# Kernel optimization log

Measured on AMD Instinct MI355X. Metric: run time of the kernel, lower is better.

## Reference

```python
import jax, jax.numpy as jnp
import numpy as np

DT_MIN, DT_MAX = 1e-3, 1e-1
LN_EPS = 1e-5


def layernorm(x, w, b):
    mu = jnp.mean(x, axis=-1, keepdims=True)
    var = jnp.mean(jnp.square(x - mu), axis=-1, keepdims=True)
    return (x - mu) * jax.lax.rsqrt(var + LN_EPS) * w + b


def _scan(Lam_bar, Bu, reverse=False):
    # Lam_bar: (P,) complex64; Bu: (B, L, P) complex64
    A = jnp.broadcast_to(Lam_bar, Bu.shape)

    def binop(e_i, e_j):
        a_i, b_i = e_i
        a_j, b_j = e_j
        return a_j * a_i, a_j * b_i + b_j

    _, xs = jax.lax.associative_scan(binop, (A, Bu), axis=1, reverse=reverse)
    return xs  # (B, L, P)


def s5_ssm(u, Lambda_re, Lambda_im, log_step, B_re, B_im, C_re, C_im, D):
    # u: (B, L, H) real. Diagonal S5 with ZOH discretization, bidirectional.
    step = jnp.exp(log_step)                          # (P,)
    Lam = (Lambda_re + 1j * Lambda_im).astype(jnp.complex64)
    Lam_bar = jnp.exp(Lam * step)                     # (P,)
    Bmat = (B_re + 1j * B_im).astype(jnp.complex64)   # (P, H)
    B_bar = ((Lam_bar - 1.0) / Lam)[:, None] * Bmat   # (P, H)
    Bu = jnp.einsum('blh,ph->blp', u.astype(jnp.complex64), B_bar)  # (B,L,P)
    xs_f = _scan(Lam_bar, Bu, reverse=False)
    xs_b = _scan(Lam_bar, Bu, reverse=True)
    xs = jnp.concatenate([xs_f, xs_b], axis=-1)       # (B, L, 2P)
    C = (C_re + 1j * C_im).astype(jnp.complex64)      # (H, 2P)
    ys = 2.0 * jnp.einsum('hp,blp->blh', C, xs).real  # conj-symmetric output
    return ys + D * u


def gelu(x):
    return jax.nn.gelu(x, approximate=False)  # torch default (erf) gelu


def s5_block(x, ln1_w, ln1_b, ln2_w, ln2_b, Lambda_re, Lambda_im, log_step,
             B_re, B_im, C_re, C_im, D, ff_enc_w, ff_dec_w):
    # attention-style half: pre-LN + S5 + gelu + residual (residual = normed input)
    fx = layernorm(x, ln1_w, ln1_b)
    res = fx
    x = gelu(s5_ssm(fx, Lambda_re, Lambda_im, log_step, B_re, B_im, C_re, C_im, D)) + res
    # FFN half: pre-LN + GEGLU + residual (residual = normed input)
    fx = layernorm(x, ln2_w, ln2_b)
    res = fx
    h = fx @ ff_enc_w.T                               # (B, L, 2*dim)
    a, g = jnp.split(h, 2, axis=-1)
    x = (a * gelu(g)) @ ff_dec_w.T + res
    return x


def setup_inputs() -> dict:
    B, L, D_IN, DIM, P = 4, 4096, 512, 1024, 512
    key = jax.random.key(0)
    ks = jax.random.split(key, 16)
    inp = {}
    inp['x'] = jax.random.normal(ks[0], (B, L, D_IN), dtype=jnp.float32)
    inp['W_in'] = jax.random.normal(ks[1], (DIM, D_IN), jnp.float32) / np.sqrt(D_IN)
    inp['W_out'] = jax.random.normal(ks[2], (D_IN, DIM), jnp.float32) / np.sqrt(DIM)
    inp['ln1_w'] = jnp.ones((DIM,), jnp.float32)
    inp['ln1_b'] = jnp.zeros((DIM,), jnp.float32)
    inp['ln2_w'] = jnp.ones((DIM,), jnp.float32)
    inp['ln2_b'] = jnp.zeros((DIM,), jnp.float32)
    inp['Lambda_re'] = -0.5 * jnp.exp(jax.random.normal(ks[3], (P,), jnp.float32))
    inp['Lambda_im'] = jnp.pi * jax.random.normal(ks[4], (P,), jnp.float32)
    inp['log_step'] = jax.random.uniform(ks[5], (P,), jnp.float32,
                                         minval=np.log(DT_MIN), maxval=np.log(DT_MAX))
    inp['B_re'] = jax.random.normal(ks[6], (P, DIM), jnp.float32) / np.sqrt(DIM)
    inp['B_im'] = jax.random.normal(ks[7], (P, DIM), jnp.float32) / np.sqrt(DIM)
    inp['C_re'] = jax.random.normal(ks[8], (DIM, 2 * P), jnp.float32) / np.sqrt(2 * P)
    inp['C_im'] = jax.random.normal(ks[9], (DIM, 2 * P), jnp.float32) / np.sqrt(2 * P)
    inp['D'] = jax.random.normal(ks[10], (DIM,), jnp.float32)
    inp['ff_enc_w'] = jax.random.normal(ks[11], (2 * DIM, DIM), jnp.float32) / np.sqrt(DIM)
    inp['ff_dec_w'] = jax.random.normal(ks[12], (DIM, DIM), jnp.float32) / np.sqrt(DIM)
    return inp


def reference(x, W_in, W_out, ln1_w, ln1_b, ln2_w, ln2_b, Lambda_re, Lambda_im,
              log_step, B_re, B_im, C_re, C_im, D, ff_enc_w, ff_dec_w):
    h = x @ W_in.T                                    # (B, L, dim)
    h = s5_block(h, ln1_w, ln1_b, ln2_w, ln2_b, Lambda_re, Lambda_im, log_step,
                 B_re, B_im, C_re, C_im, D, ff_enc_w, ff_dec_w)
    return h @ W_out.T                                # (B, L, d_input)
```

## Files before the change

kernel.cpp:

```cpp
#include <hip/hip_runtime.h>
#include <cstdint>

typedef __bf16 bf16;
typedef __bf16 bf16x2 __attribute__((ext_vector_type(2)));
typedef __bf16 bf16x4 __attribute__((ext_vector_type(4)));
typedef __bf16 bf16x8 __attribute__((ext_vector_type(8)));
typedef float f32x4 __attribute__((ext_vector_type(4)));

#define MROWS 16384
#define DIMH 1024
#define PDIM 512
#define LSEQ 4096
#define CL 16
#define NC (LSEQ / CL)

typedef const __attribute__((address_space(1))) unsigned int* gas_t;
typedef __attribute__((address_space(3))) unsigned int* las_t;

__device__ __forceinline__ float gelu_f(float x) {
  return 0.5f * x * (1.0f + erff(x * 0.70710678118654752f));
}

__global__ __launch_bounds__(256) void k_mega(
    const float* __restrict__ x, const float* __restrict__ W_in,
    const float* __restrict__ W_out, const float* __restrict__ ffe,
    const float* __restrict__ ffd, const float* __restrict__ Lre,
    const float* __restrict__ Lim, const float* __restrict__ lstep,
    const float* __restrict__ Bre, const float* __restrict__ Bim,
    const float* __restrict__ Cre, const float* __restrict__ Cim,
    bf16* __restrict__ xb, bf16* __restrict__ winb, bf16* __restrict__ woutb,
    bf16* __restrict__ ffeb, bf16* __restrict__ ffdb, bf16* __restrict__ bcat,
    bf16* __restrict__ cc, float2* __restrict__ lamb) {
  const int bid = blockIdx.x;
  const int tid = threadIdx.x;
  auto cvt4 = [&](const float* src, bf16* dst, int i4) {
    const float4 v = *(const float4*)(src + i4);
    bf16x4 o = { (bf16)v.x, (bf16)v.y, (bf16)v.z, (bf16)v.w };
    *(bf16x4*)(dst + i4) = o;
  };
  if (bid < 8192) {
    cvt4(x, xb, bid * 1024 + tid * 4);
  } else if (bid < 8704) {
    cvt4(W_in, winb, (bid - 8192) * 1024 + tid * 4);
  } else if (bid < 9216) {
    cvt4(W_out, woutb, (bid - 8704) * 1024 + tid * 4);
  } else if (bid < 11264) {
    cvt4(ffe, ffeb, (bid - 9216) * 1024 + tid * 4);
  } else if (bid < 12288) {
    cvt4(ffd, ffdb, (bid - 11264) * 1024 + tid * 4);
  } else if (bid < 12800) {
    const int i4 = (bid - 12288) * 1024 + tid * 4;
    const int p = i4 >> 10;
    const float lre = Lre[p], lim = Lim[p];
    const float st = expf(lstep[p]);
    const float er = expf(lre * st);
    const float lbr = er * cosf(lim * st);
    const float lbi = er * sinf(lim * st);
    const float ar = lbr - 1.0f, ai = lbi;
    const float d = lre * lre + lim * lim;
    const float cx = (ar * lre + ai * lim) / d;
    const float cy = (ai * lre - ar * lim) / d;
    const float4 br = *(const float4*)(Bre + i4);
    const float4 bi = *(const float4*)(Bim + i4);
    bf16x4 o1 = { (bf16)(cx * br.x - cy * bi.x), (bf16)(cx * br.y - cy * bi.y),
                  (bf16)(cx * br.z - cy * bi.z), (bf16)(cx * br.w - cy * bi.w) };
    bf16x4 o2 = { (bf16)(cx * bi.x + cy * br.x), (bf16)(cx * bi.y + cy * br.y),
                  (bf16)(cx * bi.z + cy * br.z), (bf16)(cx * bi.w + cy * br.w) };
    *(bf16x4*)(bcat + i4) = o1;
    *(bf16x4*)(bcat + i4 + PDIM * DIMH) = o2;
  } else if (bid < 14848) {
    const int i4 = (bid - 12800) * 1024 + tid * 4;
    const int n = i4 >> 11, k0 = i4 & 2047;
    const float* src;
    float sgn;
    int kk;
    if (k0 < 512)       { src = Cre + n * 1024;       sgn =  2.0f; kk = k0; }
    else if (k0 < 1024) { src = Cim + n * 1024;       sgn = -2.0f; kk = k0 - 512; }
    else if (k0 < 1536) { src = Cre + n * 1024 + 512; sgn =  2.0f; kk = k0 - 1024; }
    else                { src = Cim + n * 1024 + 512; sgn = -2.0f; kk = k0 - 1536; }
    const float4 v = *(const float4*)(src + kk);
    bf16x4 o = { (bf16)(sgn * v.x), (bf16)(sgn * v.y), (bf16)(sgn * v.z), (bf16)(sgn * v.w) };
    *(bf16x4*)(cc + i4) = o;
  } else {
    const int p = (bid - 14848) * 256 + tid;
    if (p < PDIM) {
      const float lre = Lre[p], lim = Lim[p];
      const float st = expf(lstep[p]);
      const float er = expf(lre * st);
      lamb[p] = make_float2(er * cosf(lim * st), er * sinf(lim * st));
    }
  }
}


#define VMCNT4 asm volatile("s_waitcnt vmcnt(4)" ::: "memory")
#define VMCNT0 asm volatile("s_waitcnt vmcnt(0)" ::: "memory")
#define LGKM0  asm volatile("s_waitcnt lgkmcnt(0)" ::: "memory")
#define SCHED0 __builtin_amdgcn_sched_barrier(0)
#define BAR    __builtin_amdgcn_s_barrier()

#define PHASE(slot, kh, STAGE_STMT, WAIT_STMT)                                 \
  {                                                                            \
    ldB(slot, kh, bfr);                                                        \
    ldA(slot, kh, afr);                                                        \
    STAGE_STMT;                                                                \
    SCHED0;                                                                    \
    BAR;                                                                       \
    LGKM0;                                                                     \
    SCHED0;                                                                    \
    __builtin_amdgcn_s_setprio(1);                                             \
    _Pragma("unroll")                                                          \
    for (int m = 0; m < 4; ++m)                                                \
      _Pragma("unroll")                                                        \
      for (int n = 0; n < 4; ++n)                                              \
        acc[m][n] = __builtin_amdgcn_mfma_f32_16x16x32_bf16(                   \
            afr[m], bfr[n], acc[m][n], 0, 0, 0);                               \
    __builtin_amdgcn_s_setprio(0);                                             \
    SCHED0;                                                                    \
    WAIT_STMT;                                                                 \
    BAR;                                                                       \
  }

template <int EPI>
__global__ __launch_bounds__(256, 2) void k_gemm(const bf16* __restrict__ A,
                                                 const bf16* __restrict__ W,
                                                 float* __restrict__ Cf,
                                                 bf16* __restrict__ Cb,
                                                 const bf16* __restrict__ auxb,
                                                 int K, int N, int nbnl) {
  extern __shared__ char lds[];
  const int q = (int)gridDim.x >> 3;
  const int s = ((int)blockIdx.x & 7) * q + ((int)blockIdx.x >> 3);
  const int bm = s >> nbnl;
  const int bn = s & ((1 << nbnl) - 1);
  const int tid = threadIdx.x;
  const int lane = tid & 63;
  const int wave = tid >> 6;
  const int wr = wave >> 1;
  const int wc = wave & 1;

  const size_t arow0 = (size_t)bm * 128;
  const size_t wrow0 = (size_t)bn * 128;
  const int srow = tid >> 2;
  const int schunk = (tid & 3) ^ ((tid >> 3) & 3);
  const int wbase = wave << 10;

  f32x4 acc[4][4];
#pragma unroll
  for (int i = 0; i < 4; ++i)
#pragma unroll
    for (int j = 0; j < 4; ++j) acc[i][j] = (f32x4){0.f, 0.f, 0.f, 0.f};

  auto stage = [&](int slot, int kh, int kt) {
    const int kcol = kt * 64 + kh * 32 + schunk * 8;
    {
      char* base = lds + slot * 16384 + kh * 8192;
      __builtin_amdgcn_global_load_lds(
          (gas_t)(A + (arow0 + srow) * (size_t)K + kcol), (las_t)(base + wbase), 16, 0, 0);
      __builtin_amdgcn_global_load_lds(
          (gas_t)(A + (arow0 + 64 + srow) * (size_t)K + kcol), (las_t)(base + 4096 + wbase), 16, 0, 0);
    }
    {
      char* base = lds + 32768 + slot * 16384 + kh * 8192;
      __builtin_amdgcn_global_load_lds(
          (gas_t)(W + (wrow0 + srow) * (size_t)K + kcol), (las_t)(base + wbase), 16, 0, 0);
      __builtin_amdgcn_global_load_lds(
          (gas_t)(W + (wrow0 + 64 + srow) * (size_t)K + kcol), (las_t)(base + 4096 + wbase), 16, 0, 0);
    }
  };

  auto ldA = [&](int slot, int kh, bf16x8* af) {
#pragma unroll
    for (int m = 0; m < 4; ++m) {
      const int row = wr * 64 + m * 16 + (lane & 15);
      const int pc = (lane >> 4) ^ ((row >> 1) & 3);
      af[m] = *(const bf16x8*)(lds + slot * 16384 + kh * 8192 + row * 64 + pc * 16);
    }
  };
  auto ldB = [&](int slot, int kh, bf16x8* bf) {
#pragma unroll
    for (int n = 0; n < 4; ++n) {
      const int row = wc * 64 + n * 16 + (lane & 15);
      const int pc = (lane >> 4) ^ ((row >> 1) & 3);
      bf[n] = *(const bf16x8*)(lds + 32768 + slot * 16384 + kh * 8192 + row * 64 + pc * 16);
    }
  };

  bf16x8 afr[4], bfr[4];

  stage(0, 0, 0);
  stage(0, 1, 0);
  stage(1, 0, 1);
  VMCNT4;
  BAR;

  const int NT = K >> 7;
  for (int t = 0; t < NT; ++t) {
    const int nl = (t + 1 < NT);
    PHASE(0, 0, stage(1, 1, 2 * t + 1), (void)0);
    if (nl) { PHASE(0, 1, stage(0, 0, 2 * t + 2), VMCNT4); }
    else    { PHASE(0, 1, (void)0, VMCNT0); }
    PHASE(1, 0, if (nl) stage(0, 1, 2 * t + 2), (void)0);
    if (nl) { PHASE(1, 1, stage(1, 0, 2 * t + 3), VMCNT4); }
    else    { PHASE(1, 1, (void)0, (void)0); }
  }

  const int n0 = (int)wrow0 + wc * 64 + (lane & 15);
  const size_t m0 = arow0 + wr * 64 + ((lane >> 4) << 2);
#pragma unroll
  for (int mi = 0; mi < 4; ++mi)
#pragma unroll
    for (int n = 0; n < 4; ++n) {
      const size_t mb = m0 + mi * 16;
      const int nn = n0 + n * 16;
#pragma unroll
      for (int r = 0; r < 4; ++r) {
        const size_t idx = (mb + r) * (size_t)N + nn;
        const float v = acc[mi][n][r];
        if constexpr (EPI == 0) {
          Cf[idx] = v;
        } else if constexpr (EPI == 1) {
          Cb[idx] = (bf16)((float)auxb[idx] * gelu_f(v));
        } else if constexpr (EPI == 2) {
          Cb[idx] = (bf16)(v + (float)auxb[idx]);
        } else {
          Cb[idx] = (bf16)v;
        }
      }
    }
}

__global__ __launch_bounds__(256) void k_ln(const bf16* __restrict__ X,
                                            const float* __restrict__ w,
                                            const float* __restrict__ bb,
                                            bf16* __restrict__ Yb) {
  const int m = blockIdx.x;
  const int tid = threadIdx.x;
  const bf16x4 v4 = *(const bf16x4*)(X + (size_t)m * DIMH + tid * 4);
  const float v0 = (float)v4[0], v1 = (float)v4[1], v2 = (float)v4[2], v3 = (float)v4[3];
  float s = v0 + v1 + v2 + v3;
  float s2 = v0 * v0 + v1 * v1 + v2 * v2 + v3 * v3;
#pragma unroll
  for (int off = 32; off > 0; off >>= 1) { s += __shfl_down(s, off); s2 += __shfl_down(s2, off); }
  __shared__ float rs[4], rq[4];
  if ((tid & 63) == 0) { rs[tid >> 6] = s; rq[tid >> 6] = s2; }
  __syncthreads();
  s = rs[0] + rs[1] + rs[2] + rs[3];
  s2 = rq[0] + rq[1] + rq[2] + rq[3];
  const float mu = s * (1.0f / DIMH);
  const float inv = rsqrtf(s2 * (1.0f / DIMH) - mu * mu + 1e-5f);
  const float4 wv = ((const float4*)w)[tid];
  const float4 bv = ((const float4*)bb)[tid];
  bf16x4 ob = { (bf16)((v0 - mu) * inv * wv.x + bv.x), (bf16)((v1 - mu) * inv * wv.y + bv.y),
                (bf16)((v2 - mu) * inv * wv.z + bv.z), (bf16)((v3 - mu) * inv * wv.w + bv.w) };
  *(bf16x4*)(Yb + (size_t)m * DIMH + tid * 4) = ob;
}

__global__ __launch_bounds__(256) void k_ln2e(const bf16* __restrict__ YS,
                                              bf16* FXE,
                                              const float* __restrict__ Dv,
                                              const float* __restrict__ w,
                                              const float* __restrict__ bb) {
  const int m = blockIdx.x;
  const int tid = threadIdx.x;
  const bf16x4 ys4 = *(const bf16x4*)(YS + (size_t)m * DIMH + tid * 4);
  const bf16x4 fx4 = *(const bf16x4*)(FXE + (size_t)m * DIMH + tid * 4);
  const float4 dv = ((const float4*)Dv)[tid];
  const float f0 = (float)fx4[0], f1 = (float)fx4[1], f2 = (float)fx4[2], f3 = (float)fx4[3];
  const float t0 = gelu_f((float)ys4[0] + dv.x * f0) + f0;
  const float t1 = gelu_f((float)ys4[1] + dv.y * f1) + f1;
  const float t2 = gelu_f((float)ys4[2] + dv.z * f2) + f2;
  const float t3 = gelu_f((float)ys4[3] + dv.w * f3) + f3;
  float s = t0 + t1 + t2 + t3;
  float s2 = t0 * t0 + t1 * t1 + t2 * t2 + t3 * t3;
#pragma unroll
  for (int off = 32; off > 0; off >>= 1) { s += __shfl_down(s, off); s2 += __shfl_down(s2, off); }
  __shared__ float rs[4], rq[4];
  if ((tid & 63) == 0) { rs[tid >> 6] = s; rq[tid >> 6] = s2; }
  __syncthreads();
  s = rs[0] + rs[1] + rs[2] + rs[3];
  s2 = rq[0] + rq[1] + rq[2] + rq[3];
  const float mu = s * (1.0f / DIMH);
  const float inv = rsqrtf(s2 * (1.0f / DIMH) - mu * mu + 1e-5f);
  const float4 wv = ((const float4*)w)[tid];
  const float4 bv = ((const float4*)bb)[tid];
  bf16x4 ob = { (bf16)((t0 - mu) * inv * wv.x + bv.x), (bf16)((t1 - mu) * inv * wv.y + bv.y),
                (bf16)((t2 - mu) * inv * wv.z + bv.z), (bf16)((t3 - mu) * inv * wv.w + bv.w) };
  *(bf16x4*)(FXE + (size_t)m * DIMH + tid * 4) = ob;
}

__global__ __launch_bounds__(256) void k_scanA(const bf16* __restrict__ Bu,
                                               const float2* __restrict__ lamb,
                                               float2* __restrict__ carry) {
  const int bc = blockIdx.x;
  const int b = bc >> 8, c = bc & (NC - 1);
  const int t = threadIdx.x;
  const size_t rbase = ((size_t)b * LSEQ + (size_t)c * CL) * DIMH;
  float2 re[CL], im[CL];
#pragma unroll
  for (int i = 0; i < CL; ++i) {
    const bf16x2 r2 = *(const bf16x2*)(Bu + rbase + (size_t)i * DIMH + 2 * t);
    const bf16x2 i2 = *(const bf16x2*)(Bu + rbase + (size_t)i * DIMH + PDIM + 2 * t);
    re[i] = make_float2((float)r2[0], (float)r2[1]);
    im[i] = make_float2((float)i2[0], (float)i2[1]);
  }
  const float2 l0 = lamb[2 * t];
  const float2 l1 = lamb[2 * t + 1];
  const size_t cb = ((size_t)bc * 2) * PDIM;
  {
    float s0r = 0.f, s0i = 0.f, s1r = 0.f, s1i = 0.f;
#pragma unroll
    for (int i = 0; i < CL; ++i) {
      float nr = l0.x * s0r - l0.y * s0i + re[i].x;
      float ni = l0.x * s0i + l0.y * s0r + im[i].x;
      s0r = nr; s0i = ni;
      nr = l1.x * s1r - l1.y * s1i + re[i].y;
      ni = l1.x * s1i + l1.y * s1r + im[i].y;
      s1r = nr; s1i = ni;
    }
    carry[cb + 2 * t]     = make_float2(s0r, s0i);
    carry[cb + 2 * t + 1] = make_float2(s1r, s1i);
  }
  {
    float s0r = 0.f, s0i = 0.f, s1r = 0.f, s1i = 0.f;
#pragma unroll
    for (int i = CL - 1; i >= 0; --i) {
      float nr = l0.x * s0r - l0.y * s0i + re[i].x;
      float ni = l0.x * s0i + l0.y * s0r + im[i].x;
      s0r = nr; s0i = ni;
      nr = l1.x * s1r - l1.y * s1i + re[i].y;
      ni = l1.x * s1i + l1.y * s1r + im[i].y;
      s1r = nr; s1i = ni;
    }
    carry[cb + PDIM + 2 * t]     = make_float2(s0r, s0i);
    carry[cb + PDIM + 2 * t + 1] = make_float2(s1r, s1i);
  }
}

__global__ __launch_bounds__(256) void k_scanB(const float2* __restrict__ carry,
                                               const float2* __restrict__ lamb,
                                               float2* __restrict__ seed) {
  const int b = blockIdx.x;
  const int t = threadIdx.x;
  const float2 l0 = lamb[2 * t], l1 = lamb[2 * t + 1];
  float L0r = l0.x, L0i = l0.y, L1r = l1.x, L1i = l1.y;
#pragma unroll
  for (int q = 0; q < 4; ++q) {
    float tr = L0r * L0r - L0i * L0i; L0i = 2.f * L0r * L0i; L0r = tr;
    tr = L1r * L1r - L1i * L1i; L1i = 2.f * L1r * L1i; L1r = tr;
  }
  float S0r = 0.f, S0i = 0.f, S1r = 0.f, S1i = 0.f;
  for (int c = 0; c < NC; ++c) {
    const size_t base = (((size_t)b * NC + c) * 2) * PDIM;
    const float2 c0 = carry[base + 2 * t];
    const float2 c1 = carry[base + 2 * t + 1];
    seed[base + 2 * t]     = make_float2(S0r, S0i);
    seed[base + 2 * t + 1] = make_float2(S1r, S1i);
    float nr = L0r * S0r - L0i * S0i + c0.x;
    float ni = L0r * S0i + L0i * S0r + c0.y;
    S0r = nr; S0i = ni;
    nr = L1r * S1r - L1i * S1i + c1.x;
    ni = L1r * S1i + L1i * S1r + c1.y;
    S1r = nr; S1i = ni;
  }
  S0r = 0.f; S0i = 0.f; S1r = 0.f; S1i = 0.f;
  for (int c = NC - 1; c >= 0; --c) {
    const size_t base = (((size_t)b * NC + c) * 2) * PDIM + PDIM;
    const float2 c0 = carry[base + 2 * t];
    const float2 c1 = carry[base + 2 * t + 1];
    seed[base + 2 * t]     = make_float2(S0r, S0i);
    seed[base + 2 * t + 1] = make_float2(S1r, S1i);
    float nr = L0r * S0r - L0i * S0i + c0.x;
    float ni = L0r * S0i + L0i * S0r + c0.y;
    S0r = nr; S0i = ni;
    nr = L1r * S1r - L1i * S1i + c1.x;
    ni = L1r * S1i + L1i * S1r + c1.y;
    S1r = nr; S1i = ni;
  }
}

__global__ __launch_bounds__(256) void k_scanC(const bf16* __restrict__ Bu,
                                               const float2* __restrict__ lamb,
                                               const float2* __restrict__ seed,
                                               bf16* __restrict__ xs) {
  const int bc = blockIdx.x;
  const int b = bc >> 8, c = bc & (NC - 1);
  const int t = threadIdx.x;
  const size_t rbase = ((size_t)b * LSEQ + (size_t)c * CL) * DIMH;
  float2 re[CL], im[CL];
#pragma unroll
  for (int i = 0; i < CL; ++i) {
    const bf16x2 r2 = *(const bf16x2*)(Bu + rbase + (size_t)i * DIMH + 2 * t);
    const bf16x2 i2 = *(const bf16x2*)(Bu + rbase + (size_t)i * DIMH + PDIM + 2 * t);
    re[i] = make_float2((float)r2[0], (float)r2[1]);
    im[i] = make_float2((float)i2[0], (float)i2[1]);
  }
  const float2 l0 = lamb[2 * t];
  const float2 l1 = lamb[2 * t + 1];
  const size_t sb = ((size_t)bc * 2) * PDIM;
  const size_t obase = ((size_t)b * LSEQ + (size_t)c * CL) * 2048;
  {
    const float2 s0 = seed[sb + 2 * t];
    const float2 s1 = seed[sb + 2 * t + 1];
    float s0r = s0.x, s0i = s0.y, s1r = s1.x, s1i = s1.y;
#pragma unroll
    for (int i = 0; i < CL; ++i) {
      float nr = l0.x * s0r - l0.y * s0i + re[i].x;
      float ni = l0.x * s0i + l0.y * s0r + im[i].x;
      s0r = nr; s0i = ni;
      nr = l1.x * s1r - l1.y * s1i + re[i].y;
      ni = l1.x * s1i + l1.y * s1r + im[i].y;
      s1r = nr; s1i = ni;
      bf16x2 wr2 = { (bf16)s0r, (bf16)s1r };
      bf16x2 wi2 = { (bf16)s0i, (bf16)s1i };
      *(bf16x2*)(xs + obase + (size_t)i * 2048 + 2 * t) = wr2;
      *(bf16x2*)(xs + obase + (size_t)i * 2048 + PDIM + 2 * t) = wi2;
    }
  }
  {
    const float2 s0 = seed[sb + PDIM + 2 * t];
    const float2 s1 = seed[sb + PDIM + 2 * t + 1];
    float s0r = s0.x, s0i = s0.y, s1r = s1.x, s1i = s1.y;
#pragma unroll
    for (int i = CL - 1; i >= 0; --i) {
      float nr = l0.x * s0r - l0.y * s0i + re[i].x;
      float ni = l0.x * s0i + l0.y * s0r + im[i].x;
      s0r = nr; s0i = ni;
      nr = l1.x * s1r - l1.y * s1i + re[i].y;
      ni = l1.x * s1i + l1.y * s1r + im[i].y;
      s1r = nr; s1i = ni;
      bf16x2 wr2 = { (bf16)s0r, (bf16)s1r };
      bf16x2 wi2 = { (bf16)s0i, (bf16)s1i };
      *(bf16x2*)(xs + obase + (size_t)i * 2048 + 1024 + 2 * t) = wr2;
      *(bf16x2*)(xs + obase + (size_t)i * 2048 + 1536 + 2 * t) = wi2;
    }
  }
}

extern "C" void kernel_launch(void* const* d_in, const int* in_sizes, int n_in,
                              void* d_out, int out_size, void* d_ws, size_t ws_size,
                              hipStream_t stream) {
  const float* x    = (const float*)d_in[0];
  const float* W_in = (const float*)d_in[1];
  const float* W_out= (const float*)d_in[2];
  const float* ln1w = (const float*)d_in[3];
  const float* ln1b = (const float*)d_in[4];
  const float* ln2w = (const float*)d_in[5];
  const float* ln2b = (const float*)d_in[6];
  const float* Lre  = (const float*)d_in[7];
  const float* Lim  = (const float*)d_in[8];
  const float* lstep= (const float*)d_in[9];
  const float* Bre  = (const float*)d_in[10];
  const float* Bim  = (const float*)d_in[11];
  const float* Cre  = (const float*)d_in[12];
  const float* Cim  = (const float*)d_in[13];
  const float* Dv   = (const float*)d_in[14];
  const float* ffe  = (const float*)d_in[15];
  const float* ffd  = (const float*)d_in[16];
  float* out = (float*)d_out;
  char* ws = (char*)d_ws;

  bf16* winb   = (bf16*)(ws);
  bf16* woutb  = (bf16*)(ws + (1u << 20));
  bf16* bcat   = (bf16*)(ws + (2u << 20));
  bf16* ccomb  = (bf16*)(ws + (4u << 20));
  bf16* ffeb   = (bf16*)(ws + (8u << 20));
  bf16* ffdb   = (bf16*)(ws + (12u << 20));
  float2* lamb = (float2*)(ws + (14u << 20));
  bf16* E      = (bf16*)(ws + (16u << 20));
  bf16* hb     = (bf16*)(ws + (48u << 20));
  bf16* Bub    = (bf16*)(ws + (48u << 20));
  bf16* ysb    = (bf16*)(ws + (48u << 20));
  bf16* x3b    = (bf16*)(ws + (48u << 20));
  bf16* xsb    = (bf16*)(ws + (80u << 20));
  bf16* a_b    = (bf16*)(ws + (80u << 20));
  bf16* G      = (bf16*)(ws + (112u << 20));
  float2* carry = (float2*)(ws + (144u << 20));
  float2* seed  = (float2*)(ws + (152u << 20));

  static bool attr_done = false;
  if (!attr_done) {
    hipFuncSetAttribute((const void*)&k_gemm<0>, hipFuncAttributeMaxDynamicSharedMemorySize, 65536);
    hipFuncSetAttribute((const void*)&k_gemm<1>, hipFuncAttributeMaxDynamicSharedMemorySize, 65536);
    hipFuncSetAttribute((const void*)&k_gemm<2>, hipFuncAttributeMaxDynamicSharedMemorySize, 65536);
    hipFuncSetAttribute((const void*)&k_gemm<3>, hipFuncAttributeMaxDynamicSharedMemorySize, 65536);
    attr_done = true;
  }

  k_mega<<<14850, 256, 0, stream>>>(x, W_in, W_out, ffe, ffd, Lre, Lim, lstep,
                                    Bre, Bim, Cre, Cim,
                                    E, winb, woutb, ffeb, ffdb, bcat, ccomb, lamb);

  k_gemm<3><<<1024, 256, 65536, stream>>>(E, winb, nullptr, hb, nullptr, 512, 1024, 3);
  k_ln<<<16384, 256, 0, stream>>>(hb, ln1w, ln1b, E);
  k_gemm<3><<<1024, 256, 65536, stream>>>(E, bcat, nullptr, Bub, nullptr, 1024, 1024, 3);
  k_scanA<<<4 * NC, 256, 0, stream>>>(Bub, lamb, carry);
  k_scanB<<<4, 256, 0, stream>>>(carry, lamb, seed);
  k_scanC<<<4 * NC, 256, 0, stream>>>(Bub, lamb, seed, xsb);
  k_gemm<3><<<1024, 256, 65536, stream>>>(xsb, ccomb, nullptr, ysb, nullptr, 2048, 1024, 3);
  k_ln2e<<<16384, 256, 0, stream>>>(ysb, E, Dv, ln2w, ln2b);
  k_gemm<3><<<1024, 256, 65536, stream>>>(E, ffeb, nullptr, a_b, nullptr, 1024, 1024, 3);
  k_gemm<1><<<1024, 256, 65536, stream>>>(E, ffeb + (size_t)1024 * 1024, nullptr, G, a_b, 1024, 1024, 3);
  k_gemm<2><<<1024, 256, 65536, stream>>>(G, ffdb, nullptr, x3b, E, 1024, 1024, 3);
  k_gemm<0><<<512, 256, 65536, stream>>>(x3b, woutb, out, nullptr, nullptr, 1024, 512, 2);
}
```

Before: 449.5 us.

## Restructure GEMM to 3-buffer ring for higher occupancy, add 256x256 tile GEMM for C-projection

The generic GEMM moves from a 4-slot double-kh pipeline with 64KB LDS to a 3-buffer ring of 32-wide K slices using 48KB LDS, and raises launch bounds to 3 blocks per CU so more waves can hide latency. A new 512-thread 256x256-tile GEMM with 128KB LDS handles the K=2048 C-projection to improve operand reuse. The ring uses one barrier per K step instead of two per phase, which risks less latency hiding per block and more register pressure at the higher occupancy target.

```diff
diff --git a/kernel.cpp b/kernel.cpp
--- a/kernel.cpp
+++ b/kernel.cpp
@@ -92,37 +92,14 @@
   }
 }
 
-
 #define VMCNT4 asm volatile("s_waitcnt vmcnt(4)" ::: "memory")
 #define VMCNT0 asm volatile("s_waitcnt vmcnt(0)" ::: "memory")
 #define LGKM0  asm volatile("s_waitcnt lgkmcnt(0)" ::: "memory")
 #define SCHED0 __builtin_amdgcn_sched_barrier(0)
 #define BAR    __builtin_amdgcn_s_barrier()
 
-#define PHASE(slot, kh, STAGE_STMT, WAIT_STMT)                                 \
-  {                                                                            \
-    ldB(slot, kh, bfr);                                                        \
-    ldA(slot, kh, afr);                                                        \
-    STAGE_STMT;                                                                \
-    SCHED0;                                                                    \
-    BAR;                                                                       \
-    LGKM0;                                                                     \
-    SCHED0;                                                                    \
-    __builtin_amdgcn_s_setprio(1);                                             \
-    _Pragma("unroll")                                                          \
-    for (int m = 0; m < 4; ++m)                                                \
-      _Pragma("unroll")                                                        \
-      for (int n = 0; n < 4; ++n)                                              \
-        acc[m][n] = __builtin_amdgcn_mfma_f32_16x16x32_bf16(                   \
-            afr[m], bfr[n], acc[m][n], 0, 0, 0);                               \
-    __builtin_amdgcn_s_setprio(0);                                             \
-    SCHED0;                                                                    \
-    WAIT_STMT;                                                                 \
-    BAR;                                                                       \
-  }
-
 template <int EPI>
-__global__ __launch_bounds__(256, 2) void k_gemm(const bf16* __restrict__ A,
+__global__ __launch_bounds__(256, 3) void k_gemm(const bf16* __restrict__ A,
                                                  const bf16* __restrict__ W,
                                                  float* __restrict__ Cf,
                                                  bf16* __restrict__ Cb,
@@ -151,58 +128,64 @@
 #pragma unroll
     for (int j = 0; j < 4; ++j) acc[i][j] = (f32x4){0.f, 0.f, 0.f, 0.f};
 
-  auto stage = [&](int slot, int kh, int kt) {
-    const int kcol = kt * 64 + kh * 32 + schunk * 8;
-    {
-      char* base = lds + slot * 16384 + kh * 8192;
-      __builtin_amdgcn_global_load_lds(
-          (gas_t)(A + (arow0 + srow) * (size_t)K + kcol), (las_t)(base + wbase), 16, 0, 0);
-      __builtin_amdgcn_global_load_lds(
-          (gas_t)(A + (arow0 + 64 + srow) * (size_t)K + kcol), (las_t)(base + 4096 + wbase), 16, 0, 0);
-    }
-    {
-      char* base = lds + 32768 + slot * 16384 + kh * 8192;
-      __builtin_amdgcn_global_load_lds(
-          (gas_t)(W + (wrow0 + srow) * (size_t)K + kcol), (las_t)(base + wbase), 16, 0, 0);
-      __builtin_amdgcn_global_load_lds(
-          (gas_t)(W + (wrow0 + 64 + srow) * (size_t)K + kcol), (las_t)(base + 4096 + wbase), 16, 0, 0);
-    }
+  auto stage = [&](int buf, int ui) {
+    const int kcol = ui * 32 + schunk * 8;
+    char* ba = lds + buf * 16384;
+    __builtin_amdgcn_global_load_lds(
+        (gas_t)(A + (arow0 + srow) * (size_t)K + kcol), (las_t)(ba + wbase), 16, 0, 0);
+    __builtin_amdgcn_global_load_lds(
+        (gas_t)(A + (arow0 + 64 + srow) * (size_t)K + kcol), (las_t)(ba + 4096 + wbase), 16, 0, 0);
+    char* bb = ba + 8192;
+    __builtin_amdgcn_global_load_lds(
+        (gas_t)(W + (wrow0 + srow) * (size_t)K + kcol), (las_t)(bb + wbase), 16, 0, 0);
+    __builtin_amdgcn_global_load_lds(
+        (gas_t)(W + (wrow0 + 64 + srow) * (size_t)K + kcol), (las_t)(bb + 4096 + wbase), 16, 0, 0);
   };
 
-  auto ldA = [&](int slot, int kh, bf16x8* af) {
+  auto ldA = [&](int buf, bf16x8* af) {
 #pragma unroll
     for (int m = 0; m < 4; ++m) {
       const int row = wr * 64 + m * 16 + (lane & 15);
       const int pc = (lane >> 4) ^ ((row >> 1) & 3);
-      af[m] = *(const bf16x8*)(lds + slot * 16384 + kh * 8192 + row * 64 + pc * 16);
+      af[m] = *(const bf16x8*)(lds + buf * 16384 + row * 64 + pc * 16);
     }
   };
-  auto ldB = [&](int slot, int kh, bf16x8* bf) {
+  auto ldB = [&](int buf, bf16x8* bf) {
 #pragma unroll
     for (int n = 0; n < 4; ++n) {
       const int row = wc * 64 + n * 16 + (lane & 15);
       const int pc = (lane >> 4) ^ ((row >> 1) & 3);
-      bf[n] = *(const bf16x8*)(lds + 32768 + slot * 16384 + kh * 8192 + row * 64 + pc * 16);
+      bf[n] = *(const bf16x8*)(lds + buf * 16384 + 8192 + row * 64 + pc * 16);
     }
   };
 
   bf16x8 afr[4], bfr[4];
 
-  stage(0, 0, 0);
-  stage(0, 1, 0);
-  stage(1, 0, 1);
+  stage(0, 0);
+  stage(1, 1);
   VMCNT4;
   BAR;
 
-  const int NT = K >> 7;
-  for (int t = 0; t < NT; ++t) {
-    const int nl = (t + 1 < NT);
-    PHASE(0, 0, stage(1, 1, 2 * t + 1), (void)0);
-    if (nl) { PHASE(0, 1, stage(0, 0, 2 * t + 2), VMCNT4); }
-    else    { PHASE(0, 1, (void)0, VMCNT0); }
-    PHASE(1, 0, if (nl) stage(0, 1, 2 * t + 2), (void)0);
-    if (nl) { PHASE(1, 1, stage(1, 0, 2 * t + 3), VMCNT4); }
-    else    { PHASE(1, 1, (void)0, (void)0); }
+  const int NU = K >> 5;
+  int buf = 0, sbuf = 2;
+  for (int u = 0; u < NU; ++u) {
+    ldB(buf, bfr);
+    ldA(buf, afr);
+    if (u + 2 < NU) stage(sbuf, u + 2);
+    LGKM0; SCHED0;
+    __builtin_amdgcn_s_setprio(1);
+#pragma unroll
+    for (int m = 0; m < 4; ++m)
+#pragma unroll
+      for (int n = 0; n < 4; ++n)
+        acc[m][n] = __builtin_amdgcn_mfma_f32_16x16x32_bf16(afr[m], bfr[n], acc[m][n], 0, 0, 0);
+    __builtin_amdgcn_s_setprio(0);
+    SCHED0;
+    if (u + 2 < NU) { VMCNT4; }
+    else if (u + 1 < NU) { VMCNT0; }
+    BAR;
+    buf = (buf == 2) ? 0 : buf + 1;
+    sbuf = (sbuf == 2) ? 0 : sbuf + 1;
   }
 
   const int n0 = (int)wrow0 + wc * 64 + (lane & 15);
@@ -223,6 +206,137 @@
           Cb[idx] = (bf16)((float)auxb[idx] * gelu_f(v));
         } else if constexpr (EPI == 2) {
           Cb[idx] = (bf16)(v + (float)auxb[idx]);
+        } else {
+          Cb[idx] = (bf16)v;
+        }
+      }
+    }
+}
+
+#define PHASE2(slot, kh, mh, LOADB, STAGE_STMT, WAIT_STMT)                     \
+  {                                                                            \
+    if (LOADB) ldB(slot, kh, bfr);                                             \
+    ldA(slot, kh, mh, afr);                                                    \
+    STAGE_STMT;                                                                \
+    SCHED0;                                                                    \
+    BAR;                                                                       \
+    LGKM0;                                                                     \
+    SCHED0;                                                                    \
+    __builtin_amdgcn_s_setprio(1);                                             \
+    _Pragma("unroll")                                                          \
+    for (int m = 0; m < 4; ++m)                                                \
+      _Pragma("unroll")                                                        \
+      for (int n = 0; n < 4; ++n)                                              \
+        acc[(mh) * 4 + m][n] = __builtin_amdgcn_mfma_f32_16x16x32_bf16(        \
+            afr[m], bfr[n], acc[(mh) * 4 + m][n], 0, 0, 0);                    \
+    __builtin_amdgcn_s_setprio(0);                                             \
+    SCHED0;                                                                    \
+    WAIT_STMT;                                                                 \
+    BAR;                                                                       \
+  }
+
+template <int EPI>
+__global__ __launch_bounds__(512, 2) void k_gemm2(const bf16* __restrict__ A,
+                                                  const bf16* __restrict__ W,
+                                                  float* __restrict__ Cf,
+                                                  bf16* __restrict__ Cb,
+                                                  const bf16* __restrict__ auxb,
+                                                  int K, int N, int nbnl) {
+  extern __shared__ char lds[];
+  const int q = (int)gridDim.x >> 3;
+  const int s = ((int)blockIdx.x & 7) * q + ((int)blockIdx.x >> 3);
+  const int bm = s >> nbnl;
+  const int bn = s & ((1 << nbnl) - 1);
+  const int tid = threadIdx.x;
+  const int lane = tid & 63;
+  const int wave = tid >> 6;
+  const int wr = wave >> 2;
+  const int wc = wave & 3;
+
+  const size_t arow0 = (size_t)bm * 256;
+  const size_t wrow0 = (size_t)bn * 256;
+  const int srow = tid >> 2;
+  const int schunk = (tid & 3) ^ ((tid >> 3) & 3);
+  const int wbase = wave << 10;
+
+  f32x4 acc[8][4];
+#pragma unroll
+  for (int i = 0; i < 8; ++i)
+#pragma unroll
+    for (int j = 0; j < 4; ++j) acc[i][j] = (f32x4){0.f, 0.f, 0.f, 0.f};
+
+  auto stage = [&](int slot, int kh, int kt) {
+    const int kcol = kt * 64 + kh * 32 + schunk * 8;
+    {
+      char* base = lds + slot * 32768 + kh * 16384;
+      __builtin_amdgcn_global_load_lds(
+          (gas_t)(A + (arow0 + srow) * (size_t)K + kcol), (las_t)(base + wbase), 16, 0, 0);
+      __builtin_amdgcn_global_load_lds(
+          (gas_t)(A + (arow0 + 128 + srow) * (size_t)K + kcol), (las_t)(base + 8192 + wbase), 16, 0, 0);
+    }
+    {
+      char* base = lds + 65536 + slot * 32768 + kh * 16384;
+      __builtin_amdgcn_global_load_lds(
+          (gas_t)(W + (wrow0 + srow) * (size_t)K + kcol), (las_t)(base + wbase), 16, 0, 0);
+      __builtin_amdgcn_global_load_lds(
+          (gas_t)(W + (wrow0 + 128 + srow) * (size_t)K + kcol), (las_t)(base + 8192 + wbase), 16, 0, 0);
+    }
+  };
+
+  auto ldA = [&](int slot, int kh, int mh, bf16x8* af) {
+#pragma unroll
+    for (int m = 0; m < 4; ++m) {
+      const int row = wr * 128 + mh * 64 + m * 16 + (lane & 15);
+      const int pc = (lane >> 4) ^ ((row >> 1) & 3);
+      af[m] = *(const bf16x8*)(lds + slot * 32768 + kh * 16384 + row * 64 + pc * 16);
+    }
+  };
+  auto ldB = [&](int slot, int kh, bf16x8* bf) {
+#pragma unroll
+    for (int n = 0; n < 4; ++n) {
+      const int row = wc * 64 + n * 16 + (lane & 15);
+      const int pc = (lane >> 4) ^ ((row >> 1) & 3);
+      bf[n] = *(const bf16x8*)(lds + 65536 + slot * 32768 + kh * 16384 + row * 64 + pc * 16);
+    }
+  };
+
+  bf16x8 afr[4], bfr[4];
+
+  stage(0, 0, 0);
+  stage(0, 1, 0);
+  stage(1, 0, 1);
+  VMCNT4;
+  BAR;
+
+  const int NT = K >> 7;
+  for (int t = 0; t < NT; ++t) {
+    const int nl = (t + 1 < NT);
+    PHASE2(0, 0, 0, 1, stage(1, 1, 2 * t + 1), (void)0);
+    PHASE2(0, 0, 1, 0, (void)0, (void)0);
+    PHASE2(0, 1, 0, 1, if (nl) stage(0, 0, 2 * t + 2), (void)0);
+    if (nl) { PHASE2(0, 1, 1, 0, (void)0, VMCNT4); }
+    else    { PHASE2(0, 1, 1, 0, (void)0, VMCNT0); }
+    PHASE2(1, 0, 0, 1, if (nl) stage(0, 1, 2 * t + 2), (void)0);
+    PHASE2(1, 0, 1, 0, (void)0, (void)0);
+    PHASE2(1, 1, 0, 1, if (nl) stage(1, 0, 2 * t + 3), (void)0);
+    if (nl) { PHASE2(1, 1, 1, 0, (void)0, VMCNT4); }
+    else    { PHASE2(1, 1, 1, 0, (void)0, (void)0); }
+  }
+
+  const int n0 = (int)wrow0 + wc * 64 + (lane & 15);
+  const size_t m0 = arow0 + wr * 128 + ((lane >> 4) << 2);
+#pragma unroll
+  for (int mi = 0; mi < 8; ++mi)
+#pragma unroll
+    for (int n = 0; n < 4; ++n) {
+      const size_t mb = m0 + mi * 16;
+      const int nn = n0 + n * 16;
+#pragma unroll
+      for (int r = 0; r < 4; ++r) {
+        const size_t idx = (mb + r) * (size_t)N + nn;
+        const float v = acc[mi][n][r];
+        if constexpr (EPI == 0) {
+          Cf[idx] = v;
         } else {
           Cb[idx] = (bf16)v;
         }
@@ -480,10 +594,11 @@
 
   static bool attr_done = false;
   if (!attr_done) {
-    hipFuncSetAttribute((const void*)&k_gemm<0>, hipFuncAttributeMaxDynamicSharedMemorySize, 65536);
-    hipFuncSetAttribute((const void*)&k_gemm<1>, hipFuncAttributeMaxDynamicSharedMemorySize, 65536);
-    hipFuncSetAttribute((const void*)&k_gemm<2>, hipFuncAttributeMaxDynamicSharedMemorySize, 65536);
-    hipFuncSetAttribute((const void*)&k_gemm<3>, hipFuncAttributeMaxDynamicSharedMemorySize, 65536);
+    hipFuncSetAttribute((const void*)&k_gemm<0>, hipFuncAttributeMaxDynamicSharedMemorySize, 49152);
+    hipFuncSetAttribute((const void*)&k_gemm<1>, hipFuncAttributeMaxDynamicSharedMemorySize, 49152);
+    hipFuncSetAttribute((const void*)&k_gemm<2>, hipFuncAttributeMaxDynamicSharedMemorySize, 49152);
+    hipFuncSetAttribute((const void*)&k_gemm<3>, hipFuncAttributeMaxDynamicSharedMemorySize, 49152);
+    hipFuncSetAttribute((const void*)&k_gemm2<3>, hipFuncAttributeMaxDynamicSharedMemorySize, 131072);
     attr_done = true;
   }
 
@@ -491,16 +606,16 @@
                                     Bre, Bim, Cre, Cim,
                                     E, winb, woutb, ffeb, ffdb, bcat, ccomb, lamb);
 
-  k_gemm<3><<<1024, 256, 65536, stream>>>(E, winb, nullptr, hb, nullptr, 512, 1024, 3);
+  k_gemm<3><<<1024, 256, 49152, stream>>>(E, winb, nullptr, hb, nullptr, 512, 1024, 3);
   k_ln<<<16384, 256, 0, stream>>>(hb, ln1w, ln1b, E);
-  k_gemm<3><<<1024, 256, 65536, stream>>>(E, bcat, nullptr, Bub, nullptr, 1024, 1024, 3);
+  k_gemm<3><<<1024, 256, 49152, stream>>>(E, bcat, nullptr, Bub, nullptr, 1024, 1024, 3);
   k_scanA<<<4 * NC, 256, 0, stream>>>(Bub, lamb, carry);
   k_scanB<<<4, 256, 0, stream>>>(carry, lamb, seed);
   k_scanC<<<4 * NC, 256, 0, stream>>>(Bub, lamb, seed, xsb);
-  k_gemm<3><<<1024, 256, 65536, stream>>>(xsb, ccomb, nullptr, ysb, nullptr, 2048, 1024, 3);
+  k_gemm2<3><<<256, 512, 131072, stream>>>(xsb, ccomb, nullptr, ysb, nullptr, 2048, 1024, 2);
   k_ln2e<<<16384, 256, 0, stream>>>(ysb, E, Dv, ln2w, ln2b);
-  k_gemm<3><<<1024, 256, 65536, stream>>>(E, ffeb, nullptr, a_b, nullptr, 1024, 1024, 3);
-  k_gemm<1><<<1024, 256, 65536, stream>>>(E, ffeb + (size_t)1024 * 1024, nullptr, G, a_b, 1024, 1024, 3);
-  k_gemm<2><<<1024, 256, 65536, stream>>>(G, ffdb, nullptr, x3b, E, 1024, 1024, 3);
-  k_gemm<0><<<512, 256, 65536, stream>>>(x3b, woutb, out, nullptr, nullptr, 1024, 512, 2);
-}
+  k_gemm<3><<<1024, 256, 49152, stream>>>(E, ffeb, nullptr, a_b, nullptr, 1024, 1024, 3);
+  k_gemm<1><<<1024, 256, 49152, stream>>>(E, ffeb + (size_t)1024 * 1024, nullptr, G, a_b, 1024, 1024, 3);
+  k_gemm<2><<<1024, 256, 49152, stream>>>(G, ffdb, nullptr, x3b, E, 1024, 1024, 3);
+  k_gemm<0><<<512, 256, 49152, stream>>>(x3b, woutb, out, nullptr, nullptr, 1024, 512, 2);
+}
```

Measured after the change: 449.5 us. Within noise of the previous version (-0.0%).
